# Performance work log

Measured on AMD Instinct MI355X. Metric: run time of the kernel, lower is better.

The kernel has to match this reference:

```python
import jax, jax.numpy as jnp
import numpy as np

DECAY = 0.99
EPSILON = 1e-05
CODEBOOK_SIZE = 1024


def setup_inputs() -> dict:
    key = jax.random.key(0)
    k1, k2, k3 = jax.random.split(key, 3)
    B, T, D, K = 8, 4096, 128, CODEBOOK_SIZE
    return {
        "x": jax.random.normal(k1, (B, T, D), dtype=jnp.float32),
        "embed": jax.random.normal(k2, (K, D), dtype=jnp.float32),
        "cluster_size": jnp.ones((K,), dtype=jnp.float32),
        "embed_avg": jax.random.normal(k3, (K, D), dtype=jnp.float32),
    }


def reference(x, embed, cluster_size, embed_avg):
    shape = x.shape
    K, D = embed.shape
    flat = x.reshape(-1, D)  # (N, D)

    dist = 2.0 * (flat @ embed.T) - jnp.sum(flat * flat, axis=1, keepdims=True) \
           - jnp.sum(embed * embed, axis=1)[None, :]  # (N, K)
    embed_ind_flat = jnp.argmax(dist, axis=-1)  # (N,) int
    embed_ind = embed_ind_flat.reshape(shape[:-1])
    quantize = embed[embed_ind]  # dequantize via gather, (B, T, D)

    # training EMA updates (one-hot scatter expressed as segment sums)
    counts = jax.ops.segment_sum(jnp.ones_like(embed_ind_flat, dtype=x.dtype),
                                 embed_ind_flat, num_segments=K)  # == onehot.sum(0)
    embed_sum = jax.ops.segment_sum(flat, embed_ind_flat, num_segments=K)  # == (x.T @ onehot).T

    new_cluster_size = cluster_size * DECAY + (1.0 - DECAY) * counts
    new_embed_avg = embed_avg * DECAY + (1.0 - DECAY) * embed_sum

    total = new_cluster_size.sum()
    smoothed = (new_cluster_size + EPSILON) / (total + K * EPSILON) * total
    new_embed = new_embed_avg / smoothed[:, None]

    return quantize, embed_ind, new_cluster_size, new_embed_avg, new_embed
```

## Files before the change

kernel.cpp:

```cpp
#include <hip/hip_runtime.h>

#define NROWS 32768
#define DDIM  128
#define KCODES 1024
#define DECAY 0.99f
#define OMD   0.01f
#define EPS   1e-5f

typedef __attribute__((ext_vector_type(8))) short short8;
typedef __attribute__((ext_vector_type(4))) float f32x4;

#define WS_COUNTS 0
#define WS_OFFS   1024
#define WS_CURSOR 2048
#define WS_INV    3072
#define WS_EN2H   4096
#define WS_BUCKET 5120

__device__ __forceinline__ unsigned short f2bf(float f) {
  union { float f; unsigned int u; } cv; cv.f = f;
  unsigned int u = cv.u;
  return (unsigned short)((u + 0x7fffu + ((u >> 16) & 1u)) >> 16);
}

__global__ __launch_bounds__(256) void pack_x(const float* __restrict__ x,
                                              ushort* __restrict__ xpack) {
  const int tid = threadIdx.x;
  const int w = tid >> 6, lane = tid & 63;
  const int mt = blockIdx.x * 4 + w;
  const int m = lane & 15, q = lane >> 4;
  const int row = mt * 16 + m;
  const float* xp = x + (size_t)row * DDIM + q * 8;
  #pragma unroll
  for (int kb = 0; kb < 4; ++kb) {
    float4 v0 = *(const float4*)(xp + kb * 32);
    float4 v1 = *(const float4*)(xp + kb * 32 + 4);
    float v[8] = {v0.x, v0.y, v0.z, v0.w, v1.x, v1.y, v1.z, v1.w};
    unsigned int h[8], l[8];
    #pragma unroll
    for (int j = 0; j < 8; ++j) {
      h[j] = f2bf(v[j]);
      float fh = __uint_as_float(h[j] << 16);
      l[j] = f2bf(v[j] - fh);
    }
    uint4 ph, pl;
    ph.x = h[0] | (h[1] << 16); ph.y = h[2] | (h[3] << 16);
    ph.z = h[4] | (h[5] << 16); ph.w = h[6] | (h[7] << 16);
    pl.x = l[0] | (l[1] << 16); pl.y = l[2] | (l[3] << 16);
    pl.z = l[4] | (l[5] << 16); pl.w = l[6] | (l[7] << 16);
    *(uint4*)(xpack + (((size_t)mt * 8 + kb) * 64 + lane) * 8)     = ph;
    *(uint4*)(xpack + (((size_t)mt * 8 + kb + 4) * 64 + lane) * 8) = pl;
  }
}

__global__ __launch_bounds__(256) void pack_e(const float* __restrict__ embed,
                                              ushort* __restrict__ epack,
                                              float* __restrict__ en2h) {
  const int tid = threadIdx.x;
  const int w = tid >> 6, lane = tid & 63;
  const int nt = blockIdx.x * 4 + w;
  const int m = lane & 15, q = lane >> 4;
  const int row = nt * 16 + m;
  const float* ep = embed + (size_t)row * DDIM + q * 8;
  float ss = 0.f;
  #pragma unroll
  for (int kb = 0; kb < 4; ++kb) {
    float4 v0 = *(const float4*)(ep + kb * 32);
    float4 v1 = *(const float4*)(ep + kb * 32 + 4);
    float v[8] = {v0.x, v0.y, v0.z, v0.w, v1.x, v1.y, v1.z, v1.w};
    unsigned int h[8], l[8];
    #pragma unroll
    for (int j = 0; j < 8; ++j) {
      ss += v[j] * v[j];
      h[j] = f2bf(v[j]);
      float fh = __uint_as_float(h[j] << 16);
      l[j] = f2bf(v[j] - fh);
    }
    uint4 ph, pl;
    ph.x = h[0] | (h[1] << 16); ph.y = h[2] | (h[3] << 16);
    ph.z = h[4] | (h[5] << 16); ph.w = h[6] | (h[7] << 16);
    pl.x = l[0] | (l[1] << 16); pl.y = l[2] | (l[3] << 16);
    pl.z = l[4] | (l[5] << 16); pl.w = l[6] | (l[7] << 16);
    *(uint4*)(epack + (((size_t)nt * 8 + kb) * 64 + lane) * 8)     = ph;
    *(uint4*)(epack + (((size_t)nt * 8 + kb + 4) * 64 + lane) * 8) = pl;
  }
  ss += __shfl_xor(ss, 16, 64);
  ss += __shfl_xor(ss, 32, 64);
  if (q == 0) en2h[row] = 0.5f * ss;
}

__global__ __launch_bounds__(256, 2) void vq_mfma(
    const short8* __restrict__ xp8, const short8* __restrict__ ep8,
    const float* __restrict__ en2h,
    float* __restrict__ counts, float* __restrict__ out_ind) {
  __shared__ unsigned long long keys[4][64];
  const int tid = threadIdx.x;
  const int w = tid >> 6, lane = tid & 63;
  const int c = lane & 15, q = lane >> 4;
  const int mt0 = blockIdx.x * 4;
  const int nt0 = w * 16;

  short8 a[4][8];
  #pragma unroll
  for (int t = 0; t < 4; ++t)
    #pragma unroll
    for (int kb = 0; kb < 8; ++kb)
      a[t][kb] = xp8[((size_t)(mt0 + t) * 8 + kb) * 64 + lane];

  float bestv[16]; int besti[16];
  #pragma unroll
  for (int i = 0; i < 16; ++i) { bestv[i] = -3.4e38f; besti[i] = 0; }

  for (int ch = 0; ch < 16; ++ch) {
    const int nt = nt0 + ch;
    short8 st[8];
    #pragma unroll
    for (int j = 0; j < 8; ++j)
      st[j] = ep8[((size_t)nt * 8 + j) * 64 + lane];
    const float nh = en2h[nt * 16 + c];
    f32x4 acc[4];
    #pragma unroll
    for (int t = 0; t < 4; ++t) acc[t] = (f32x4){0.f, 0.f, 0.f, 0.f};
    #pragma unroll
    for (int t = 0; t < 4; ++t) {
      #pragma unroll
      for (int kb = 0; kb < 4; ++kb)
        acc[t] = __builtin_amdgcn_mfma_f32_16x16x32_bf16(a[t][kb], st[kb], acc[t], 0, 0, 0);
      #pragma unroll
      for (int kb = 0; kb < 4; ++kb)
        acc[t] = __builtin_amdgcn_mfma_f32_16x16x32_bf16(a[t][4 + kb], st[kb], acc[t], 0, 0, 0);
      #pragma unroll
      for (int kb = 0; kb < 4; ++kb)
        acc[t] = __builtin_amdgcn_mfma_f32_16x16x32_bf16(a[t][kb], st[4 + kb], acc[t], 0, 0, 0);
    }
    const int code = nt * 16 + c;
    #pragma unroll
    for (int t = 0; t < 4; ++t)
      #pragma unroll
      for (int r = 0; r < 4; ++r) {
        float s = acc[t][r] - nh;
        int i = t * 4 + r;
        if (s > bestv[i]) { bestv[i] = s; besti[i] = code; }
      }
  }

  #pragma unroll
  for (int off = 1; off < 16; off <<= 1) {
    #pragma unroll
    for (int i = 0; i < 16; ++i) {
      float ov = __shfl_xor(bestv[i], off, 64);
      int   oi = __shfl_xor(besti[i], off, 64);
      if (ov > bestv[i] || (ov == bestv[i] && oi < besti[i])) {
        bestv[i] = ov; besti[i] = oi;
      }
    }
  }
  if (c == 0) {
    #pragma unroll
    for (int t = 0; t < 4; ++t)
      #pragma unroll
      for (int r = 0; r < 4; ++r) {
        unsigned u = __float_as_uint(bestv[t * 4 + r]);
        unsigned su = (u & 0x80000000u) ? ~u : (u | 0x80000000u);
        keys[w][t * 16 + q * 4 + r] =
            ((unsigned long long)su << 32) |
            (unsigned long long)(0xFFFFFFFFu - (unsigned)besti[t * 4 + r]);
      }
  }
  __syncthreads();
  if (tid < 64) {
    unsigned long long k0 = keys[0][tid], k1 = keys[1][tid];
    unsigned long long k2 = keys[2][tid], k3 = keys[3][tid];
    unsigned long long k = k0 > k1 ? k0 : k1;
    if (k2 > k) k = k2;
    if (k3 > k) k = k3;
    int code = (int)(0xFFFFFFFFu - (unsigned)(k & 0xFFFFFFFFull));
    out_ind[blockIdx.x * 64 + tid] = (float)code;
    unsafeAtomicAdd(counts + code, 1.0f);
  }
}

__global__ void scan_fin(const float* __restrict__ counts, const float* __restrict__ cs,
                         int* __restrict__ offs, int* __restrict__ cursor,
                         float* __restrict__ out_ncs, float* __restrict__ inv) {
  __shared__ float wtot[16];
  __shared__ float ctot[16];
  int tid = threadIdx.x;
  int lane = tid & 63, w = tid >> 6;
  float cnum = counts[tid];
  float cv = cs[tid];
  float s = cnum;
  #pragma unroll
  for (int off = 1; off < 64; off <<= 1) {
    float v = __shfl_up(s, off, 64);
    if (lane >= off) s += v;
  }
  float r2 = cv;
  #pragma unroll
  for (int off = 32; off > 0; off >>= 1) r2 += __shfl_down(r2, off, 64);
  if (lane == 63) wtot[w] = s;
  if (lane == 0)  ctot[w] = r2;
  __syncthreads();
  if (tid < 16) {
    float v = wtot[tid];
    #pragma unroll
    for (int off = 1; off < 16; off <<= 1) {
      float p = __shfl_up(v, off, 64);
      if (tid >= off) v += p;
    }
    wtot[tid] = v;
    float t2 = ctot[tid];
    #pragma unroll
    for (int off = 8; off > 0; off >>= 1) t2 += __shfl_down(t2, off, 64);
    if (tid == 0) ctot[0] = t2;
  }
  __syncthreads();
  float prefix = (w > 0) ? wtot[w - 1] : 0.f;
  int excl = (int)(s + prefix) - (int)cnum;
  offs[tid] = excl;
  cursor[tid] = excl;
  float ncs = cv * DECAY + OMD * cnum;
  out_ncs[tid] = ncs;
  float total = ctot[0] * DECAY + OMD * (float)NROWS;
  inv[tid] = (total + (float)KCODES * EPS) / ((ncs + EPS) * total);
}

__global__ void scatter_rows(const float* __restrict__ out_ind,
                             int* __restrict__ cursor, int* __restrict__ bucket) {
  int row = blockIdx.x * 256 + threadIdx.x;
  int code = (int)out_ind[row];
  int pos = atomicAdd(cursor + code, 1);
  bucket[pos] = row;
}

__global__ __launch_bounds__(256) void q_write(
    const float* __restrict__ out_ind, const float* __restrict__ embed,
    float* __restrict__ out_q) {
  int gid = blockIdx.x * 256 + threadIdx.x;
  int row = gid >> 5, c4 = gid & 31;
  int code = (int)out_ind[row];
  *(float4*)(out_q + (size_t)gid * 4) =
      *(const float4*)(embed + (size_t)code * DDIM + c4 * 4);
}

__global__ __launch_bounds__(256) void esum_fin(
    const int* __restrict__ bucket, const int* __restrict__ offs,
    const float* __restrict__ counts, const float* __restrict__ x,
    const float* __restrict__ ea, const float* __restrict__ inv,
    float* __restrict__ out_nea, float* __restrict__ out_ne) {
  __shared__ float4 part[512];
  const int code = blockIdx.x;
  const int t = threadIdx.x;
  const int c8 = t & 15;
  const int h = t >> 4;
  const int start = offs[code];
  const int cnt = (int)counts[code];
  float4 a0 = {0.f, 0.f, 0.f, 0.f}, a1 = {0.f, 0.f, 0.f, 0.f};
  int i = h;
  for (; i + 16 < cnt; i += 32) {
    int rowA = bucket[start + i];
    int rowB = bucket[start + i + 16];
    const float* pa = x + (size_t)rowA * DDIM + c8 * 8;
    const float* pb = x + (size_t)rowB * DDIM + c8 * 8;
    float4 xa0 = *(const float4*)(pa), xa1 = *(const float4*)(pa + 4);
    float4 xb0 = *(const float4*)(pb), xb1 = *(const float4*)(pb + 4);
    a0.x += xa0.x + xb0.x; a0.y += xa0.y + xb0.y; a0.z += xa0.z + xb0.z; a0.w += xa0.w + xb0.w;
    a1.x += xa1.x + xb1.x; a1.y += xa1.y + xb1.y; a1.z += xa1.z + xb1.z; a1.w += xa1.w + xb1.w;
  }
  for (; i < cnt; i += 16) {
    int row = bucket[start + i];
    const float* pa = x + (size_t)row * DDIM + c8 * 8;
    float4 xa0 = *(const float4*)(pa), xa1 = *(const float4*)(pa + 4);
    a0.x += xa0.x; a0.y += xa0.y; a0.z += xa0.z; a0.w += xa0.w;
    a1.x += xa1.x; a1.y += xa1.y; a1.z += xa1.z; a1.w += xa1.w;
  }
  part[h * 32 + c8 * 2]     = a0;
  part[h * 32 + c8 * 2 + 1] = a1;
  __syncthreads();
  if (t < 32) {
    float4 s = part[t];
    #pragma unroll
    for (int hh = 1; hh < 16; ++hh) {
      float4 p = part[hh * 32 + t];
      s.x += p.x; s.y += p.y; s.z += p.z; s.w += p.w;
    }
    float iv = inv[code];
    int base = code * DDIM + t * 4;
    float4 a = *(const float4*)(ea + base);
    float4 nea;
    nea.x = a.x * DECAY + OMD * s.x; nea.y = a.y * DECAY + OMD * s.y;
    nea.z = a.z * DECAY + OMD * s.z; nea.w = a.w * DECAY + OMD * s.w;
    *(float4*)(out_nea + base) = nea;
    float4 ne;
    ne.x = nea.x * iv; ne.y = nea.y * iv; ne.z = nea.z * iv; ne.w = nea.w * iv;
    *(float4*)(out_ne + base) = ne;
  }
}

extern "C" void kernel_launch(void* const* d_in, const int* in_sizes, int n_in,
                              void* d_out, int out_size, void* d_ws, size_t ws_size,
                              hipStream_t stream) {
  const float* x     = (const float*)d_in[0];
  const float* embed = (const float*)d_in[1];
  const float* cs    = (const float*)d_in[2];
  const float* ea    = (const float*)d_in[3];

  float* out     = (float*)d_out;
  float* out_q   = out;
  float* out_ind = out_q + 4194304;
  float* out_ncs = out_ind + 32768;
  float* out_nea = out_ncs + 1024;
  float* out_ne  = out_nea + 131072;

  float* ws     = (float*)d_ws;
  float* counts = ws + WS_COUNTS;
  int*   offs   = (int*)(ws + WS_OFFS);
  int*   cursor = (int*)(ws + WS_CURSOR);
  float* inv    = ws + WS_INV;
  float* en2h   = ws + WS_EN2H;
  int*   bucket = (int*)(ws + WS_BUCKET);

  ushort* xpack = (ushort*)out_q;
  ushort* epack = (ushort*)out_nea;

  hipMemsetAsync(counts, 0, KCODES * sizeof(float), stream);
  pack_x<<<512, 256, 0, stream>>>(x, xpack);
  pack_e<<<16, 256, 0, stream>>>(embed, epack, en2h);
  vq_mfma<<<NROWS / 64, 256, 0, stream>>>((const short8*)xpack, (const short8*)epack,
                                          en2h, counts, out_ind);
  scan_fin<<<1, 1024, 0, stream>>>(counts, cs, offs, cursor, out_ncs, inv);
  scatter_rows<<<NROWS / 256, 256, 0, stream>>>(out_ind, cursor, bucket);
  q_write<<<(NROWS * 32) / 256, 256, 0, stream>>>(out_ind, embed, out_q);
  esum_fin<<<KCODES, 256, 0, stream>>>(bucket, offs, counts, x, ea, inv,
                                       out_nea, out_ne);
}
```

Before: 180.5 us.

## Fuse x bf16 split into vq_mfma and quantize gather into esum kernel

Drops the pack_x kernel: vq_mfma now reads fp32 x directly and does the hi/lo bf16 split in registers before the MFMA loop. Also drops q_write: the per-code esum kernel, which already walks each code's rows, loads that code's embedding once and writes it to every assigned row of out_q. This removes two launches and the round trip of the packed x buffer through memory. In exchange vq_mfma does more conversion work and uses more registers (waves_per_eu changed), and the out_q writes become scattered per bucket and unevenly spread across code blocks.

Result: slower. 184.8 us (+2.4%).

```diff
diff --git a/kernel.cpp b/kernel.cpp
--- a/kernel.cpp
+++ b/kernel.cpp
@@ -21,36 +21,6 @@
   union { float f; unsigned int u; } cv; cv.f = f;
   unsigned int u = cv.u;
   return (unsigned short)((u + 0x7fffu + ((u >> 16) & 1u)) >> 16);
-}
-
-__global__ __launch_bounds__(256) void pack_x(const float* __restrict__ x,
-                                              ushort* __restrict__ xpack) {
-  const int tid = threadIdx.x;
-  const int w = tid >> 6, lane = tid & 63;
-  const int mt = blockIdx.x * 4 + w;
-  const int m = lane & 15, q = lane >> 4;
-  const int row = mt * 16 + m;
-  const float* xp = x + (size_t)row * DDIM + q * 8;
-  #pragma unroll
-  for (int kb = 0; kb < 4; ++kb) {
-    float4 v0 = *(const float4*)(xp + kb * 32);
-    float4 v1 = *(const float4*)(xp + kb * 32 + 4);
-    float v[8] = {v0.x, v0.y, v0.z, v0.w, v1.x, v1.y, v1.z, v1.w};
-    unsigned int h[8], l[8];
-    #pragma unroll
-    for (int j = 0; j < 8; ++j) {
-      h[j] = f2bf(v[j]);
-      float fh = __uint_as_float(h[j] << 16);
-      l[j] = f2bf(v[j] - fh);
-    }
-    uint4 ph, pl;
-    ph.x = h[0] | (h[1] << 16); ph.y = h[2] | (h[3] << 16);
-    ph.z = h[4] | (h[5] << 16); ph.w = h[6] | (h[7] << 16);
-    pl.x = l[0] | (l[1] << 16); pl.y = l[2] | (l[3] << 16);
-    pl.z = l[4] | (l[5] << 16); pl.w = l[6] | (l[7] << 16);
-    *(uint4*)(xpack + (((size_t)mt * 8 + kb) * 64 + lane) * 8)     = ph;
-    *(uint4*)(xpack + (((size_t)mt * 8 + kb + 4) * 64 + lane) * 8) = pl;
-  }
 }
 
 __global__ __launch_bounds__(256) void pack_e(const float* __restrict__ embed,
@@ -89,8 +59,10 @@
   if (q == 0) en2h[row] = 0.5f * ss;
 }
 
-__global__ __launch_bounds__(256, 2) void vq_mfma(
-    const short8* __restrict__ xp8, const short8* __restrict__ ep8,
+__global__ __launch_bounds__(256)
+__attribute__((amdgpu_waves_per_eu(2, 2)))
+void vq_mfma(
+    const float* __restrict__ x, const short8* __restrict__ ep8,
     const float* __restrict__ en2h,
     float* __restrict__ counts, float* __restrict__ out_ind) {
   __shared__ unsigned long long keys[4][64];
@@ -102,10 +74,25 @@
 
   short8 a[4][8];
   #pragma unroll
-  for (int t = 0; t < 4; ++t)
-    #pragma unroll
-    for (int kb = 0; kb < 8; ++kb)
-      a[t][kb] = xp8[((size_t)(mt0 + t) * 8 + kb) * 64 + lane];
+  for (int t = 0; t < 4; ++t) {
+    const float* xp = x + (size_t)((mt0 + t) * 16 + c) * DDIM + q * 8;
+    #pragma unroll
+    for (int kb = 0; kb < 4; ++kb) {
+      float4 v0 = *(const float4*)(xp + kb * 32);
+      float4 v1 = *(const float4*)(xp + kb * 32 + 4);
+      float v[8] = {v0.x, v0.y, v0.z, v0.w, v1.x, v1.y, v1.z, v1.w};
+      short8 hh, ll;
+      #pragma unroll
+      for (int j = 0; j < 8; ++j) {
+        unsigned int hv = f2bf(v[j]);
+        hh[j] = (short)hv;
+        float fh = __uint_as_float(hv << 16);
+        ll[j] = (short)f2bf(v[j] - fh);
+      }
+      a[t][kb] = hh;
+      a[t][kb + 4] = ll;
+    }
+  }
 
   float bestv[16]; int besti[16];
   #pragma unroll
@@ -233,21 +220,12 @@
   bucket[pos] = row;
 }
 
-__global__ __launch_bounds__(256) void q_write(
-    const float* __restrict__ out_ind, const float* __restrict__ embed,
-    float* __restrict__ out_q) {
-  int gid = blockIdx.x * 256 + threadIdx.x;
-  int row = gid >> 5, c4 = gid & 31;
-  int code = (int)out_ind[row];
-  *(float4*)(out_q + (size_t)gid * 4) =
-      *(const float4*)(embed + (size_t)code * DDIM + c4 * 4);
-}
-
-__global__ __launch_bounds__(256) void esum_fin(
+__global__ __launch_bounds__(256) void esum_q_fin(
     const int* __restrict__ bucket, const int* __restrict__ offs,
     const float* __restrict__ counts, const float* __restrict__ x,
-    const float* __restrict__ ea, const float* __restrict__ inv,
-    float* __restrict__ out_nea, float* __restrict__ out_ne) {
+    const float* __restrict__ embed, const float* __restrict__ ea,
+    const float* __restrict__ inv,
+    float* __restrict__ out_q, float* __restrict__ out_nea, float* __restrict__ out_ne) {
   __shared__ float4 part[512];
   const int code = blockIdx.x;
   const int t = threadIdx.x;
@@ -255,6 +233,8 @@
   const int h = t >> 4;
   const int start = offs[code];
   const int cnt = (int)counts[code];
+  const float4 e0 = *(const float4*)(embed + (size_t)code * DDIM + c8 * 8);
+  const float4 e1 = *(const float4*)(embed + (size_t)code * DDIM + c8 * 8 + 4);
   float4 a0 = {0.f, 0.f, 0.f, 0.f}, a1 = {0.f, 0.f, 0.f, 0.f};
   int i = h;
   for (; i + 16 < cnt; i += 32) {
@@ -264,6 +244,10 @@
     const float* pb = x + (size_t)rowB * DDIM + c8 * 8;
     float4 xa0 = *(const float4*)(pa), xa1 = *(const float4*)(pa + 4);
     float4 xb0 = *(const float4*)(pb), xb1 = *(const float4*)(pb + 4);
+    float* qa = out_q + (size_t)rowA * DDIM + c8 * 8;
+    float* qb = out_q + (size_t)rowB * DDIM + c8 * 8;
+    *(float4*)(qa) = e0; *(float4*)(qa + 4) = e1;
+    *(float4*)(qb) = e0; *(float4*)(qb + 4) = e1;
     a0.x += xa0.x + xb0.x; a0.y += xa0.y + xb0.y; a0.z += xa0.z + xb0.z; a0.w += xa0.w + xb0.w;
     a1.x += xa1.x + xb1.x; a1.y += xa1.y + xb1.y; a1.z += xa1.z + xb1.z; a1.w += xa1.w + xb1.w;
   }
@@ -271,6 +255,8 @@
     int row = bucket[start + i];
     const float* pa = x + (size_t)row * DDIM + c8 * 8;
     float4 xa0 = *(const float4*)(pa), xa1 = *(const float4*)(pa + 4);
+    float* qa = out_q + (size_t)row * DDIM + c8 * 8;
+    *(float4*)(qa) = e0; *(float4*)(qa + 4) = e1;
     a0.x += xa0.x; a0.y += xa0.y; a0.z += xa0.z; a0.w += xa0.w;
     a1.x += xa1.x; a1.y += xa1.y; a1.z += xa1.z; a1.w += xa1.w;
   }
@@ -320,17 +306,13 @@
   float* en2h   = ws + WS_EN2H;
   int*   bucket = (int*)(ws + WS_BUCKET);
 
-  ushort* xpack = (ushort*)out_q;
   ushort* epack = (ushort*)out_nea;
 
   hipMemsetAsync(counts, 0, KCODES * sizeof(float), stream);
-  pack_x<<<512, 256, 0, stream>>>(x, xpack);
   pack_e<<<16, 256, 0, stream>>>(embed, epack, en2h);
-  vq_mfma<<<NROWS / 64, 256, 0, stream>>>((const short8*)xpack, (const short8*)epack,
-                                          en2h, counts, out_ind);
+  vq_mfma<<<NROWS / 64, 256, 0, stream>>>(x, (const short8*)epack, en2h, counts, out_ind);
   scan_fin<<<1, 1024, 0, stream>>>(counts, cs, offs, cursor, out_ncs, inv);
   scatter_rows<<<NROWS / 256, 256, 0, stream>>>(out_ind, cursor, bucket);
-  q_write<<<(NROWS * 32) / 256, 256, 0, stream>>>(out_ind, embed, out_q);
-  esum_fin<<<KCODES, 256, 0, stream>>>(bucket, offs, counts, x, ea, inv,
-                                       out_nea, out_ne);
-}
+  esum_q_fin<<<KCODES, 256, 0, stream>>>(bucket, offs, counts, x, embed, ea, inv,
+                                         out_q, out_nea, out_ne);
+}
```
